# Performance work log

Measured on AMD Instinct MI355X. Metric: run time of the kernel, lower is better.

Reference implementation:

```python
import jax, jax.numpy as jnp
import numpy as np

SR = 44100
PRE_EMPH = 0.97
FRAME_LEN = int(0.02 * SR)      # 882
FRAME_HOP = FRAME_LEN // 2      # 441
N_FFT = 2048
EPS = 1e-10


def setup_inputs() -> dict:
    key = jax.random.key(0)
    k1, k2 = jax.random.split(key)
    waveform = jax.random.normal(k1, (16, 441000), dtype=jnp.float32)
    # librosa mel filterbank is a fixed nonnegative (n_mels, n_fft//2+1) matrix;
    # a random surrogate keeps the math (dense matmul) identical.
    mel_filters = jax.random.uniform(k2, (60, N_FFT // 2 + 1), dtype=jnp.float32)
    return {"waveform": waveform, "mel_filters": mel_filters}


def _mfdwc(waveform, mel_filters):
    dt = waveform.dtype
    # pre-emphasis: y[0]=x[0], y[t]=x[t]-0.97*x[t-1]
    emph = jnp.concatenate(
        [waveform[:, :1], waveform[:, 1:] - PRE_EMPH * waveform[:, :-1]], axis=1)
    L = emph.shape[1]
    n_frames = 1 + (L - FRAME_LEN) // FRAME_HOP  # static
    idx = jnp.arange(n_frames)[:, None] * FRAME_HOP + jnp.arange(FRAME_LEN)[None, :]
    frames = emph[:, idx]                                   # (B, T, 882)
    window = jnp.asarray(np.hamming(FRAME_LEN), dtype=dt)   # (882,)
    windowed = frames * window
    spec = jnp.fft.rfft(windowed, n=N_FFT, axis=-1)         # (B, T, 1025) complex
    power = jnp.real(spec) ** 2 + jnp.imag(spec) ** 2       # |FFT|^2
    mel = jnp.einsum('mf,btf->btm', mel_filters, power)     # (B, T, 60)
    logmel = jnp.log(mel + EPS)
    # 1-level Haar DWT along mel axis (pywt convention, even length):
    # cA = (x_even + x_odd)/sqrt(2), cD = (x_even - x_odd)/sqrt(2)
    sq2 = jnp.sqrt(jnp.asarray(2.0, dt))
    x_even, x_odd = logmel[..., 0::2], logmel[..., 1::2]
    cA = (x_even + x_odd) / sq2                             # (B, T, 30)
    cD = (x_even - x_odd) / sq2                             # (B, T, 30)
    # delta (window=3, edge-padded): d[t] = a[clamp(t+1)] - a[clamp(t-1)]
    fwd = jnp.concatenate([cA[:, 1:], cA[:, -1:]], axis=1)
    bwd = jnp.concatenate([cA[:, :1], cA[:, :-1]], axis=1)
    delta = fwd - bwd
    feats = jnp.concatenate([cA, delta, cD], axis=-1)       # (B, T, 90)
    mean = jnp.mean(feats, axis=1)
    std = jnp.std(feats, axis=1, ddof=1)                    # torch.std unbiased
    return jnp.concatenate([mean, std], axis=1)             # (B, 180)


def reference(waveform, mel_filters):
    return _mfdwc(waveform, mel_filters)
```

## Files before the change

### kernel.cpp

```cpp
#include <hip/hip_runtime.h>
#include <hip/hip_bf16.h>
#include <math.h>

#define FRAME_LEN 882
#define FRAME_HOP 441
#define NFFT 2048
#define NFRAMES 999
#define NBATCH 16
#define NMEL 60
#define WAVE_LEN 441000
#define PRE_EMPH 0.97f
#define EPS 1e-10f
#define NROWS (NBATCH * NFRAMES)
#define KPAD 1056
#define PI_F 3.14159265358979323846f

#define PADI(i) ((i) + ((i) >> 4))

__device__ __forceinline__ float2 cadd(float2 a, float2 b){ return make_float2(a.x+b.x, a.y+b.y); }
__device__ __forceinline__ float2 csub(float2 a, float2 b){ return make_float2(a.x-b.x, a.y-b.y); }
__device__ __forceinline__ float2 cmul(float2 a, float2 b){ return make_float2(a.x*b.x - a.y*b.y, a.x*b.y + a.y*b.x); }
__device__ __forceinline__ float2 rotni(float2 z){ return make_float2(z.y, -z.x); }

__device__ __forceinline__ void dif_group8(float2* x, float2 t1) {
  const float2 C41 = make_float2(0.7071067812f, -0.7071067812f);
  float2 w0 = t1, w1 = cmul(t1, C41), w2 = rotni(w0), w3 = rotni(w1);
  float2 u, v;
  u=x[0]; v=x[4]; x[0]=cadd(u,v); x[4]=cmul(csub(u,v), w0);
  u=x[1]; v=x[5]; x[1]=cadd(u,v); x[5]=cmul(csub(u,v), w1);
  u=x[2]; v=x[6]; x[2]=cadd(u,v); x[6]=cmul(csub(u,v), w2);
  u=x[3]; v=x[7]; x[3]=cadd(u,v); x[7]=cmul(csub(u,v), w3);
  float2 t2 = cmul(t1, t1), t2r = rotni(t2);
  u=x[0]; v=x[2]; x[0]=cadd(u,v); x[2]=cmul(csub(u,v), t2);
  u=x[1]; v=x[3]; x[1]=cadd(u,v); x[3]=cmul(csub(u,v), t2r);
  u=x[4]; v=x[6]; x[4]=cadd(u,v); x[6]=cmul(csub(u,v), t2);
  u=x[5]; v=x[7]; x[5]=cadd(u,v); x[7]=cmul(csub(u,v), t2r);
  float2 t4 = cmul(t2, t2);
  u=x[0]; v=x[1]; x[0]=cadd(u,v); x[1]=cmul(csub(u,v), t4);
  u=x[2]; v=x[3]; x[2]=cadd(u,v); x[3]=cmul(csub(u,v), t4);
  u=x[4]; v=x[5]; x[4]=cadd(u,v); x[5]=cmul(csub(u,v), t4);
  u=x[6]; v=x[7]; x[6]=cadd(u,v); x[7]=cmul(csub(u,v), t4);
}

__device__ __forceinline__ void dif_radix4(float2* x) {
  float2 y0 = cadd(x[0], x[2]);
  float2 y2 = csub(x[0], x[2]);
  float2 y1 = cadd(x[1], x[3]);
  float2 t3 = csub(x[1], x[3]);
  float2 y3 = rotni(t3);
  x[0] = cadd(y0, y1); x[1] = csub(y0, y1);
  x[2] = cadd(y2, y3); x[3] = csub(y2, y3);
}

__global__ __launch_bounds__(256) void fft_pow_kernel(
    const float* __restrict__ wav, __hip_bfloat16* __restrict__ powr)
{
  __shared__ float2 lds[NFFT + (NFFT >> 4)];
  const int t  = threadIdx.x;
  const int t0 = 2 * blockIdx.x, t1f = t0 + 1;
  const bool has1 = (t1f < NFRAMES);
  const int b = blockIdx.y;
  const float* w = wav + (size_t)b * WAVE_LEN;
  const int s0 = t0 * FRAME_HOP, s1 = t1f * FRAME_HOP;

  float2 x[8];
  {
    float sB, cB, sD, cD;
    __sincosf(6.283185307179586f * (float)t / 881.0f, &sB, &cB);
    __sincosf(6.283185307179586f * 256.0f / 881.0f, &sD, &cD);
    float2 cur  = make_float2(cB, sB);
    float2 step = make_float2(cD, sD);
#pragma unroll
    for (int k = 0; k < 8; ++k) {
      int i = k * 256 + t;
      float v1 = 0.f, v2 = 0.f;
      if (i < FRAME_LEN) {
        float win = 0.54f - 0.46f * cur.x;
        int s = s0 + i;
        float e1 = (s > 0) ? (w[s] - PRE_EMPH * w[s - 1]) : w[s];
        v1 = e1 * win;
        if (has1) {
          int ss = s1 + i;
          v2 = (w[ss] - PRE_EMPH * w[ss - 1]) * win;
        }
      }
      x[k] = make_float2(v1, v2);
      cur = cmul(cur, step);
    }
  }

  {
    float sA, cA;
    __sincosf(-PI_F * (float)t / 1024.0f, &sA, &cA);
    dif_group8(x, make_float2(cA, sA));
  }
#pragma unroll
  for (int k = 0; k < 8; ++k) lds[PADI(k * 256 + t)] = x[k];
  __syncthreads();

  {
    const int q = t >> 5, r = t & 31;
#pragma unroll
    for (int k = 0; k < 8; ++k) x[k] = lds[PADI(q * 256 + k * 32 + r)];
    float sA, cA;
    __sincosf(-PI_F * (float)r / 128.0f, &sA, &cA);
    dif_group8(x, make_float2(cA, sA));
    __syncthreads();
#pragma unroll
    for (int k = 0; k < 8; ++k) lds[PADI(q * 256 + k * 32 + r)] = x[k];
  }
  __syncthreads();

  {
    const int q = t >> 2, r = t & 3;
#pragma unroll
    for (int k = 0; k < 8; ++k) x[k] = lds[PADI(q * 32 + k * 4 + r)];
    float tc = (r == 0) ? 1.0f : (r == 1) ? 0.980785280f : (r == 2) ? 0.923879533f : 0.831469612f;
    float ts = (r == 0) ? 0.0f : (r == 1) ? -0.195090322f : (r == 2) ? -0.382683432f : -0.555570233f;
    dif_group8(x, make_float2(tc, ts));
    __syncthreads();
#pragma unroll
    for (int k = 0; k < 8; ++k) lds[PADI(q * 32 + k * 4 + r)] = x[k];
  }
  __syncthreads();

  {
    float2 xa[4], xb[4];
#pragma unroll
    for (int j = 0; j < 4; ++j) {
      xa[j] = lds[PADI(4 * t + j)];
      xb[j] = lds[PADI(4 * (t + 256) + j)];
    }
    dif_radix4(xa);
    dif_radix4(xb);
    __syncthreads();
#pragma unroll
    for (int j = 0; j < 4; ++j) {
      lds[PADI(4 * t + j)] = xa[j];
      lds[PADI(4 * (t + 256) + j)] = xb[j];
    }
  }
  __syncthreads();

  const size_t row0 = (size_t)b * NFRAMES + t0;
  __hip_bfloat16* p0 = powr + row0 * KPAD;
  __hip_bfloat16* p1 = powr + (row0 + 1) * KPAD;
#pragma unroll
  for (int c = 0; c < 5; ++c) {
    int f = t + 256 * c;
    bool valid = (c < 4) || (t == 0);
    if (c == 4) f = 1024;
    if (valid) {
      int j1 = (int)(__brev((unsigned)f) >> 21);
      int j2 = (int)(__brev((unsigned)((NFFT - f) & (NFFT - 1))) >> 21);
      float2 z = lds[PADI(j1)];
      float2 y = lds[PADI(j2)];
      float f1r = z.x + y.x, f1i = z.y - y.y;
      float f2r = z.y + y.y, f2i = y.x - z.x;
      float pw1 = 0.25f * (f1r * f1r + f1i * f1i);
      float pw2 = 0.25f * (f2r * f2r + f2i * f2i);
      p0[f] = __float2bfloat16(pw1);
      if (has1) p1[f] = __float2bfloat16(pw2);
    }
  }
  if (t < KPAD - 1025) {
    p0[1025 + t] = __float2bfloat16(0.f);
    if (has1) p1[1025 + t] = __float2bfloat16(0.f);
  }
}

__global__ __launch_bounds__(256) void filtconv_kernel(
    const float* __restrict__ filt, __hip_bfloat16* __restrict__ filtb)
{
  const int m = blockIdx.x;
  for (int k = threadIdx.x; k < KPAD; k += 256) {
    float v = (m < NMEL && k < 1025) ? filt[m * 1025 + k] : 0.f;
    filtb[(size_t)m * KPAD + k] = __float2bfloat16(v);
  }
}

typedef __attribute__((ext_vector_type(8))) short short8x;
typedef __attribute__((ext_vector_type(4))) float float4x;

__global__ __launch_bounds__(256) void melgemm_kernel(
    const __hip_bfloat16* __restrict__ powr,
    const __hip_bfloat16* __restrict__ filtb,
    float* __restrict__ logmel)
{
  const int wave = threadIdx.x >> 6, lane = threadIdx.x & 63;
  const int row0 = blockIdx.x * 16;
  const int lrow = lane & 15, kgrp = lane >> 4;

  const __hip_bfloat16* ap = powr + (size_t)(row0 + lrow) * KPAD + kgrp * 8;
  const __hip_bfloat16* bp = filtb + (size_t)(wave * 16 + lrow) * KPAD + kgrp * 8;

  float4x acc = {0.f, 0.f, 0.f, 0.f};
#pragma unroll 3
  for (int kk = 0; kk < 33; ++kk) {
    short8x a = *(const short8x*)ap;
    short8x bf = *(const short8x*)bp;
    acc = __builtin_amdgcn_mfma_f32_16x16x32_bf16(a, bf, acc, 0, 0, 0);
    ap += 32; bp += 32;
  }

  const int mel = wave * 16 + (lane & 15);
  const int rsub = (lane >> 4) * 4;
  if (mel < NMEL) {
#pragma unroll
    for (int reg = 0; reg < 4; ++reg) {
      int row = row0 + rsub + reg;
      logmel[(size_t)row * NMEL + mel] = __logf(acc[reg] + EPS);
    }
  }
}

__global__ __launch_bounds__(256) void stats_kernel(
    const float* __restrict__ logmel, float* __restrict__ out)
{
  __shared__ float red[4];
  const int j   = blockIdx.x;
  const int b   = blockIdx.y;
  const int tid = threadIdx.x;
  const float* lm = logmel + (size_t)b * NFRAMES * NMEL;
  const float inv_sq2 = 0.7071067811865475f;

  float fv[4];
  int   nf = 0;
#pragma unroll
  for (int r = 0; r < 4; ++r) {
    int tt = tid + (r << 8);
    if (tt < NFRAMES) {
      float v;
      if (j < 30) {
        int m = j;
        v = (lm[tt * NMEL + 2 * m] + lm[tt * NMEL + 2 * m + 1]) * inv_sq2;
      } else if (j < 60) {
        int m  = j - 30;
        int tp = (tt + 1 > NFRAMES - 1) ? (NFRAMES - 1) : (tt + 1);
        int tm = (tt - 1 < 0) ? 0 : (tt - 1);
        float ca_p = (lm[tp * NMEL + 2 * m] + lm[tp * NMEL + 2 * m + 1]) * inv_sq2;
        float ca_m = (lm[tm * NMEL + 2 * m] + lm[tm * NMEL + 2 * m + 1]) * inv_sq2;
        v = ca_p - ca_m;
      } else {
        int m = j - 60;
        v = (lm[tt * NMEL + 2 * m] - lm[tt * NMEL + 2 * m + 1]) * inv_sq2;
      }
      fv[nf++] = v;
    }
  }

  float s = 0.f;
  for (int r = 0; r < nf; ++r) s += fv[r];
  for (int o = 32; o > 0; o >>= 1) s += __shfl_xor(s, o, 64);
  if ((tid & 63) == 0) red[tid >> 6] = s;
  __syncthreads();
  float mean = (red[0] + red[1] + red[2] + red[3]) / (float)NFRAMES;
  __syncthreads();

  float s2 = 0.f;
  for (int r = 0; r < nf; ++r) { float d = fv[r] - mean; s2 += d * d; }
  for (int o = 32; o > 0; o >>= 1) s2 += __shfl_xor(s2, o, 64);
  if ((tid & 63) == 0) red[tid >> 6] = s2;
  __syncthreads();
  float var = (red[0] + red[1] + red[2] + red[3]) / (float)(NFRAMES - 1);

  if (tid == 0) {
    out[b * 180 + j]      = mean;
    out[b * 180 + 90 + j] = sqrtf(var);
  }
}

extern "C" void kernel_launch(void* const* d_in, const int* in_sizes, int n_in,
                              void* d_out, int out_size, void* d_ws, size_t ws_size,
                              hipStream_t stream) {
  const float* wav  = (const float*)d_in[0];
  const float* filt = (const float*)d_in[1];
  float* out = (float*)d_out;

  unsigned char* ws = (unsigned char*)d_ws;
  __hip_bfloat16* powr  = (__hip_bfloat16*)(ws);
  size_t off = (size_t)NROWS * KPAD * 2;
  __hip_bfloat16* filtb = (__hip_bfloat16*)(ws + off);
  off += (size_t)64 * KPAD * 2;
  float* logmel = (float*)(ws + off);

  filtconv_kernel<<<64, 256, 0, stream>>>(filt, filtb);
  fft_pow_kernel<<<dim3((NFRAMES + 1) / 2, NBATCH), 256, 0, stream>>>(wav, powr);
  melgemm_kernel<<<NROWS / 16, 256, 0, stream>>>(powr, filtb, logmel);
  stats_kernel<<<dim3(90, NBATCH), 256, 0, stream>>>(logmel, out);
}
```

Measured before the change: 135.9 us.

## Transpose logmel to mel-major layout and split GEMM K-loop into two accumulators

The mel GEMM now writes log-mel values transposed (mel-major, frames contiguous), so each stats block reads contiguous, coalesced frame vectors instead of strided per-frame rows. The GEMM K loop is split into two independent MFMA accumulator chains, which shortens the dependency chain and lets more loads be in flight. The GEMM store becomes strided across mel rows, which may cost some write efficiency.

```diff
diff --git a/kernel.cpp b/kernel.cpp
--- a/kernel.cpp
+++ b/kernel.cpp
@@ -185,7 +185,7 @@
 __global__ __launch_bounds__(256) void melgemm_kernel(
     const __hip_bfloat16* __restrict__ powr,
     const __hip_bfloat16* __restrict__ filtb,
-    float* __restrict__ logmel)
+    float* __restrict__ logmelT)
 {
   const int wave = threadIdx.x >> 6, lane = threadIdx.x & 63;
   const int row0 = blockIdx.x * 16;
@@ -194,13 +194,21 @@
   const __hip_bfloat16* ap = powr + (size_t)(row0 + lrow) * KPAD + kgrp * 8;
   const __hip_bfloat16* bp = filtb + (size_t)(wave * 16 + lrow) * KPAD + kgrp * 8;
 
-  float4x acc = {0.f, 0.f, 0.f, 0.f};
-#pragma unroll 3
-  for (int kk = 0; kk < 33; ++kk) {
-    short8x a = *(const short8x*)ap;
-    short8x bf = *(const short8x*)bp;
-    acc = __builtin_amdgcn_mfma_f32_16x16x32_bf16(a, bf, acc, 0, 0, 0);
-    ap += 32; bp += 32;
+  float4x acc0 = {0.f, 0.f, 0.f, 0.f};
+  float4x acc1 = {0.f, 0.f, 0.f, 0.f};
+#pragma unroll 4
+  for (int kk = 0; kk < 16; ++kk) {
+    short8x a0 = *(const short8x*)(ap + kk * 32);
+    short8x b0 = *(const short8x*)(bp + kk * 32);
+    short8x a1 = *(const short8x*)(ap + (kk + 16) * 32);
+    short8x b1 = *(const short8x*)(bp + (kk + 16) * 32);
+    acc0 = __builtin_amdgcn_mfma_f32_16x16x32_bf16(a0, b0, acc0, 0, 0, 0);
+    acc1 = __builtin_amdgcn_mfma_f32_16x16x32_bf16(a1, b1, acc1, 0, 0, 0);
+  }
+  {
+    short8x a = *(const short8x*)(ap + 32 * 32);
+    short8x bf = *(const short8x*)(bp + 32 * 32);
+    acc0 = __builtin_amdgcn_mfma_f32_16x16x32_bf16(a, bf, acc0, 0, 0, 0);
   }
 
   const int mel = wave * 16 + (lane & 15);
@@ -209,57 +217,65 @@
 #pragma unroll
     for (int reg = 0; reg < 4; ++reg) {
       int row = row0 + rsub + reg;
-      logmel[(size_t)row * NMEL + mel] = __logf(acc[reg] + EPS);
+      float vv = acc0[reg] + acc1[reg];
+      logmelT[(size_t)mel * NROWS + row] = __logf(vv + EPS);
     }
   }
 }
 
 __global__ __launch_bounds__(256) void stats_kernel(
-    const float* __restrict__ logmel, float* __restrict__ out)
+    const float* __restrict__ lmT, float* __restrict__ out)
 {
   __shared__ float red[4];
   const int j   = blockIdx.x;
   const int b   = blockIdx.y;
   const int tid = threadIdx.x;
-  const float* lm = logmel + (size_t)b * NFRAMES * NMEL;
+  const int base = b * NFRAMES;
   const float inv_sq2 = 0.7071067811865475f;
-
-  float fv[4];
-  int   nf = 0;
-#pragma unroll
-  for (int r = 0; r < 4; ++r) {
-    int tt = tid + (r << 8);
-    if (tt < NFRAMES) {
-      float v;
-      if (j < 30) {
-        int m = j;
-        v = (lm[tt * NMEL + 2 * m] + lm[tt * NMEL + 2 * m + 1]) * inv_sq2;
-      } else if (j < 60) {
-        int m  = j - 30;
-        int tp = (tt + 1 > NFRAMES - 1) ? (NFRAMES - 1) : (tt + 1);
-        int tm = (tt - 1 < 0) ? 0 : (tt - 1);
-        float ca_p = (lm[tp * NMEL + 2 * m] + lm[tp * NMEL + 2 * m + 1]) * inv_sq2;
-        float ca_m = (lm[tm * NMEL + 2 * m] + lm[tm * NMEL + 2 * m + 1]) * inv_sq2;
-        v = ca_p - ca_m;
-      } else {
-        int m = j - 60;
-        v = (lm[tt * NMEL + 2 * m] - lm[tt * NMEL + 2 * m + 1]) * inv_sq2;
-      }
-      fv[nf++] = v;
-    }
-  }
-
-  float s = 0.f;
-  for (int r = 0; r < nf; ++r) s += fv[r];
-  for (int o = 32; o > 0; o >>= 1) s += __shfl_xor(s, o, 64);
+  const bool v3 = (tid < NFRAMES - 768);
+
+  float f0, f1, f2, f3;
+  if (j < 30) {
+    const float* e = lmT + (size_t)(2 * j) * NROWS + base;
+    const float* o = lmT + (size_t)(2 * j + 1) * NROWS + base;
+    f0 = (e[tid]       + o[tid])       * inv_sq2;
+    f1 = (e[tid + 256] + o[tid + 256]) * inv_sq2;
+    f2 = (e[tid + 512] + o[tid + 512]) * inv_sq2;
+    f3 = v3 ? (e[tid + 768] + o[tid + 768]) * inv_sq2 : 0.f;
+  } else if (j < 60) {
+    const int m = j - 30;
+    const float* e = lmT + (size_t)(2 * m) * NROWS + base;
+    const float* o = lmT + (size_t)(2 * m + 1) * NROWS + base;
+    auto dl = [&](int t) -> float {
+      int tp = (t + 1 > NFRAMES - 1) ? (NFRAMES - 1) : (t + 1);
+      int tm = (t - 1 < 0) ? 0 : (t - 1);
+      return ((e[tp] + o[tp]) - (e[tm] + o[tm])) * inv_sq2;
+    };
+    f0 = dl(tid);
+    f1 = dl(tid + 256);
+    f2 = dl(tid + 512);
+    f3 = v3 ? dl(tid + 768) : 0.f;
+  } else {
+    const int m = j - 60;
+    const float* e = lmT + (size_t)(2 * m) * NROWS + base;
+    const float* o = lmT + (size_t)(2 * m + 1) * NROWS + base;
+    f0 = (e[tid]       - o[tid])       * inv_sq2;
+    f1 = (e[tid + 256] - o[tid + 256]) * inv_sq2;
+    f2 = (e[tid + 512] - o[tid + 512]) * inv_sq2;
+    f3 = v3 ? (e[tid + 768] - o[tid + 768]) * inv_sq2 : 0.f;
+  }
+
+  float s = f0 + f1 + f2 + f3;
+  for (int o2 = 32; o2 > 0; o2 >>= 1) s += __shfl_xor(s, o2, 64);
   if ((tid & 63) == 0) red[tid >> 6] = s;
   __syncthreads();
   float mean = (red[0] + red[1] + red[2] + red[3]) / (float)NFRAMES;
   __syncthreads();
 
-  float s2 = 0.f;
-  for (int r = 0; r < nf; ++r) { float d = fv[r] - mean; s2 += d * d; }
-  for (int o = 32; o > 0; o >>= 1) s2 += __shfl_xor(s2, o, 64);
+  float d0 = f0 - mean, d1 = f1 - mean, d2 = f2 - mean;
+  float d3 = v3 ? (f3 - mean) : 0.f;
+  float s2 = d0 * d0 + d1 * d1 + d2 * d2 + d3 * d3;
+  for (int o2 = 32; o2 > 0; o2 >>= 1) s2 += __shfl_xor(s2, o2, 64);
   if ((tid & 63) == 0) red[tid >> 6] = s2;
   __syncthreads();
   float var = (red[0] + red[1] + red[2] + red[3]) / (float)(NFRAMES - 1);
@@ -282,10 +298,10 @@
   size_t off = (size_t)NROWS * KPAD * 2;
   __hip_bfloat16* filtb = (__hip_bfloat16*)(ws + off);
   off += (size_t)64 * KPAD * 2;
-  float* logmel = (float*)(ws + off);
+  float* logmelT = (float*)(ws + off);
 
   filtconv_kernel<<<64, 256, 0, stream>>>(filt, filtb);
   fft_pow_kernel<<<dim3((NFRAMES + 1) / 2, NBATCH), 256, 0, stream>>>(wav, powr);
-  melgemm_kernel<<<NROWS / 16, 256, 0, stream>>>(powr, filtb, logmel);
-  stats_kernel<<<dim3(90, NBATCH), 256, 0, stream>>>(logmel, out);
-}
+  melgemm_kernel<<<NROWS / 16, 256, 0, stream>>>(powr, filtb, logmelT);
+  stats_kernel<<<dim3(90, NBATCH), 256, 0, stream>>>(logmelT, out);
+}
```

New measurement: 128.3 us. 5.6% less time.
